# Performance work log

Measured on AMD Instinct MI355X. Metric: run time of the kernel, lower is better.

The kernel has to match this reference:

```python
import jax, jax.numpy as jnp
import numpy as np

B, S = 2, 4096
H, D = 8, 64      # num_heads, per-head embed_dim
W = 128           # window (even)
O = 64            # num_outputs per head
ZERO_VALUE = 0.0


def setup_inputs() -> dict:
    key = jax.random.key(0)
    kq, kk, kv, kwq, kwk, kbq, kbk, ko = jax.random.split(key, 8)
    scale = 1.0 / np.sqrt(D)
    return {
        "q": jax.random.normal(kq, (B, S, H * D), dtype=jnp.float32),
        "k": jax.random.normal(kk, (B, S, H * D), dtype=jnp.float32),
        "v": jax.random.normal(kv, (B, S, H * O), dtype=jnp.float32),
        "Wq": jax.random.normal(kwq, (D, D), dtype=jnp.float32) * scale,
        "bq": jax.random.normal(kbq, (D,), dtype=jnp.float32) * 0.02,
        "Wk": jax.random.normal(kwk, (D, D), dtype=jnp.float32) * scale,
        "bk": jax.random.normal(kbk, (D,), dtype=jnp.float32) * 0.02,
        "ocpe": jax.random.normal(ko, (W + 1, H), dtype=jnp.float32) * 0.02,
    }


def reference(q, k, v, Wq, bq, Wk, bk, ocpe):
    b, s, _ = q.shape
    p = W // 2
    assert s % W == 0
    C = s // W  # number of chunks of size `window`

    # split heads + per-head projections (nn.Linear: x @ W.T + b)
    q = q.reshape(b, s, H, D) @ Wq.T + bq
    k = k.reshape(b, s, H, D) @ Wk.T + bk
    v = v.reshape(b, s, H, O)

    # pad seq dim by window//2 on both sides (matches F.pad in source)
    qp = jnp.pad(q, ((0, 0), (p, p), (0, 0), (0, 0)))
    kp = jnp.pad(k, ((0, 0), (p, p), (0, 0), (0, 0)))
    vp = jnp.pad(v, ((0, 0), (p, p), (0, 0), (0, 0)))

    # overlapping chunks of length 2W (chunk_size=W plus 2*p halo)
    starts = jnp.arange(C) * W                 # (C,)
    loc = jnp.arange(2 * W)                    # (2W,)
    idx = starts[:, None] + loc[None, :]       # (C, 2W) indices into padded seq
    qc = qp[:, idx]                            # (B, C, 2W, H, D)
    kc = kp[:, idx]
    vc = vp[:, idx]                            # (B, C, 2W, H, O)

    scores = jnp.einsum('ncxhd,ncyhd->ncxyh', qc, kc)  # (B,C,2W,2W,H)

    diff = loc[None, :] - loc[:, None]         # j - i, (2W, 2W)
    within = jnp.abs(diff) <= p                # (2W, 2W)
    bias = jnp.where(within[:, :, None],
                     ocpe[jnp.clip(p + diff, 0, W)], 0.0)  # (2W,2W,H)
    scores = scores + bias[None, None]

    # boundary mask: global padded position must lie in [p, s+p)
    pos = starts[:, None] + loc[None, :]       # (C, 2W)
    valid = (pos >= p) & (pos < s + p)         # (C, 2W)
    mask = within[None] & valid[:, :, None] & valid[:, None, :]  # (C,2W,2W)

    scores = jnp.where(mask[None, :, :, :, None], scores, ZERO_VALUE)
    attn = jnp.tanh(scores)

    res = jnp.einsum('ncxyh,ncyhd->ncxd', attn, vc)  # (B,C,2W,O)
    out = res[:, :, p:2 * W - p].reshape(b, s, O)     # middle W rows per chunk

    # attn_flat[b,c,i,d,h] = attn[b,c, i+p, i+d, h]
    r = jnp.arange(W)
    rows = r[:, None] + p                      # (W, 1)
    cols = r[:, None] + jnp.arange(W + 1)[None]  # (W, W+1)
    attn_flat = attn[:, :, rows, cols, :]      # (B, C, W, W+1, H)
    attn_flat = attn_flat.reshape(b, s, W + 1, H)
    return attn_flat, out
```

## Files before the change

kernel.cpp:

```cpp
#include <hip/hip_runtime.h>
#include <cstddef>

#define SB 2
#define SS 4096
#define SH 8
#define SD 64
#define SP 64
#define SNO 129
#define TQ 16
#define WN 144
#define NT16 (SS/TQ)
#define SSTR 168

typedef _Float16 f16;
typedef __attribute__((ext_vector_type(8))) _Float16 f16x8;
typedef __attribute__((ext_vector_type(4))) float floatx4;

union f16frag { f16 h[8]; ushort4 u4[2]; f16x8 v; };
union pack4 { f16 h[4]; ushort4 u; };

__device__ __forceinline__ float fast_tanh(float x) {
  float e = __expf(2.0f * x);
  return 1.0f - 2.0f * __builtin_amdgcn_rcpf(e + 1.0f);
}

__device__ __forceinline__ void cvt16(const float* __restrict__ src, f16* __restrict__ dst) {
  float4 x0 = *(const float4*)(src);
  float4 x1 = *(const float4*)(src + 4);
  float4 x2 = *(const float4*)(src + 8);
  float4 x3 = *(const float4*)(src + 12);
  f16frag a, c;
  a.h[0]=(f16)x0.x; a.h[1]=(f16)x0.y; a.h[2]=(f16)x0.z; a.h[3]=(f16)x0.w;
  a.h[4]=(f16)x1.x; a.h[5]=(f16)x1.y; a.h[6]=(f16)x1.z; a.h[7]=(f16)x1.w;
  c.h[0]=(f16)x2.x; c.h[1]=(f16)x2.y; c.h[2]=(f16)x2.z; c.h[3]=(f16)x2.w;
  c.h[4]=(f16)x3.x; c.h[5]=(f16)x3.y; c.h[6]=(f16)x3.z; c.h[7]=(f16)x3.w;
  *(ushort4*)(dst)      = a.u4[0];
  *(ushort4*)(dst + 4)  = a.u4[1];
  *(ushort4*)(dst + 8)  = c.u4[0];
  *(ushort4*)(dst + 12) = c.u4[1];
}

__global__ __launch_bounds__(256) void prep_kernel(
    const float* __restrict__ q, const float* __restrict__ k, const float* __restrict__ v,
    const float* __restrict__ Wq, const float* __restrict__ bq,
    const float* __restrict__ Wk, const float* __restrict__ bk,
    f16* __restrict__ Qf, f16* __restrict__ Kf, f16* __restrict__ Vt)
{
  __shared__ f16 sWq[64*72], sWk[64*72], sQr[64*72], sKr[64*72], sVr[64*72];
  __shared__ float sbq[64], sbk[64];

  int t = threadIdx.x;
  int blk = blockIdx.x;
  int x = blk & 7, j = blk >> 3;
  int c = x*8 + (j & 7);
  int h = (j >> 3) & 7;
  int b = j >> 6;
  int s0 = c * 64;

  int dr = t >> 2, e0 = (t & 3) * 16;
  cvt16(Wq + dr*64 + e0, &sWq[dr*72 + e0]);
  cvt16(Wk + dr*64 + e0, &sWk[dr*72 + e0]);
  {
    size_t rbase = ((size_t)(b*SS + s0 + dr)) * (SH*SD) + h*SD + e0;
    cvt16(q + rbase, &sQr[dr*72 + e0]);
    cvt16(k + rbase, &sKr[dr*72 + e0]);
    cvt16(v + rbase, &sVr[dr*72 + e0]);
  }
  if (t < 64) { sbq[t] = bq[t]; sbk[t] = bk[t]; }
  __syncthreads();

  int lane = t & 63, wave = t >> 6;
  int r16 = lane & 15, g = lane >> 4;
  size_t hsbase = (size_t)(b*SH + h) * SS;

  #pragma unroll
  for (int jj = 0; jj < 4; ++jj) {
    int tt = wave + 4*jj;
    int si = tt >> 2, dj = tt & 3;
    floatx4 accq = {0.f,0.f,0.f,0.f}, acck = {0.f,0.f,0.f,0.f};
    #pragma unroll
    for (int e = 0; e < 64; e += 32) {
      f16x8 aq = *(const f16x8*)&sQr[(si*16 + r16)*72 + e + g*8];
      f16x8 ak = *(const f16x8*)&sKr[(si*16 + r16)*72 + e + g*8];
      f16x8 wq8 = *(const f16x8*)&sWq[(dj*16 + r16)*72 + e + g*8];
      f16x8 wk8 = *(const f16x8*)&sWk[(dj*16 + r16)*72 + e + g*8];
      accq = __builtin_amdgcn_mfma_f32_16x16x32_f16(aq, wq8, accq, 0, 0, 0);
      acck = __builtin_amdgcn_mfma_f32_16x16x32_f16(ak, wk8, acck, 0, 0, 0);
    }
    float biasq = sbq[dj*16 + r16];
    float biask = sbk[dj*16 + r16];
    #pragma unroll
    for (int rr = 0; rr < 4; ++rr) {
      int srow = s0 + si*16 + g*4 + rr;
      Qf[(hsbase + srow)*64 + dj*16 + r16] = (f16)(accq[rr] + biasq);
      Kf[(hsbase + srow)*64 + dj*16 + r16] = (f16)(acck[rr] + biask);
    }
  }
  {
    int d = t >> 2, p4 = t & 3, sc0 = p4 * 16;
    f16frag a, c2;
    #pragma unroll
    for (int j2 = 0; j2 < 8; ++j2) a.h[j2] = sVr[(sc0 + j2)*72 + d];
    #pragma unroll
    for (int j2 = 0; j2 < 8; ++j2) c2.h[j2] = sVr[(sc0 + 8 + j2)*72 + d];
    f16* dst = Vt + ((size_t)(b*SH + h)*64 + d)*SS + s0 + sc0;
    *(ushort4*)dst       = a.u4[0];
    *(ushort4*)(dst + 4) = a.u4[1];
    *(ushort4*)(dst + 8) = c2.u4[0];
    *(ushort4*)(dst + 12)= c2.u4[1];
  }
}

__global__ __launch_bounds__(512, 4) void attn_fused(
    const f16* __restrict__ Qf, const f16* __restrict__ Kf, const f16* __restrict__ Vt,
    const float* __restrict__ ocpe, float* __restrict__ af, float* __restrict__ outp)
{
  __shared__ f16 sPriv[SH][TQ*SSTR];
  __shared__ f16 sAF[TQ*SNO*SH];
  __shared__ float sObT[SH*SNO];

  int t = threadIdx.x;
  int lane = t & 63, wave = t >> 6;
  int r16 = lane & 15, g = lane >> 4;

  int blk = blockIdx.x;
  int x = blk & 7, j = blk >> 3;
  int t16 = x*32 + (j & 31);
  int b = j >> 5;
  int t0 = t16 * TQ, yg0 = t0 - SP;

  int h = wave;
  const f16* qb = Qf + ((size_t)(b*SH + h)*SS + t0 + r16)*64;
  f16x8 qa0 = *(const f16x8*)(qb + g*8);
  f16x8 qa1 = *(const f16x8*)(qb + 32 + g*8);

  for (int idx = t; idx < SNO*SH; idx += 512) {
    int o = idx >> 3, h2 = idx & 7;
    sObT[h2*SNO + o] = ocpe[idx];
  }
  f16* priv = &sPriv[wave][0];
  #pragma unroll
  for (int jj = 0; jj < 4; ++jj)
    priv[r16*SSTR + WN + g*4 + jj] = (f16)0.f;

  __syncthreads();

  const float* ob = &sObT[h*SNO];
  const f16* kbase = Kf + ((size_t)(b*SH + h)*SS)*64;
  floatx4 acc2[4] = {{0.f,0.f,0.f,0.f},{0.f,0.f,0.f,0.f},{0.f,0.f,0.f,0.f},{0.f,0.f,0.f,0.f}};

  bool interior = (t16 >= 4) & (t16 <= 250);

  if (interior) {
    const f16* krow = kbase + (size_t)(yg0 + r16) * 64 + g*8;
    #pragma unroll
    for (int yy = 0; yy < 9; ++yy) {
      f16x8 kb0 = *(const f16x8*)(krow + yy*1024);
      f16x8 kb1 = *(const f16x8*)(krow + yy*1024 + 32);
      floatx4 acc = {0.f,0.f,0.f,0.f};
      acc = __builtin_amdgcn_mfma_f32_16x16x32_f16(kb0, qa0, acc, 0, 0, 0);
      acc = __builtin_amdgcn_mfma_f32_16x16x32_f16(kb1, qa1, acc, 0, 0, 0);
      int y0 = yy*16 + g*4;
      int i = r16;
      pack4 pk;
      #pragma unroll
      for (int rr = 0; rr < 4; ++rr) {
        int o = y0 + rr - i;
        bool ook = (o >= 0) & (o <= 2*SP);
        f16 ah = (f16)0.f;
        if (ook) {
          ah = (f16)fast_tanh(acc[rr] + ob[o]);
          sAF[((size_t)i*SNO + o)*SH + h] = ah;
        }
        pk.h[rr] = ah;
      }
      *(ushort4*)&priv[i*SSTR + y0] = pk.u;
    }
    const f16* vrow = Vt + ((size_t)(b*SH + h)*64 + r16)*SS + yg0 + g*8;
    #pragma unroll
    for (int ks = 0; ks < 5; ++ks) {
      int yb = ks*32 + g*8;
      f16x8 a0 = *(const f16x8*)&priv[r16*SSTR + yb];
      #pragma unroll
      for (int dq = 0; dq < 4; ++dq) {
        f16x8 bv = *(const f16x8*)(vrow + (size_t)(dq*16)*SS + ks*32);
        acc2[dq] = __builtin_amdgcn_mfma_f32_16x16x32_f16(a0, bv, acc2[dq], 0, 0, 0);
      }
    }
  } else {
    #pragma unroll
    for (int yy = 0; yy < 9; ++yy) {
      int ldr = yg0 + yy*16 + r16;
      int ldc = min(max(ldr, 0), SS-1);
      const f16* kr = kbase + (size_t)ldc * 64;
      f16x8 kb0 = *(const f16x8*)(kr + g*8);
      f16x8 kb1 = *(const f16x8*)(kr + 32 + g*8);
      floatx4 acc = {0.f,0.f,0.f,0.f};
      acc = __builtin_amdgcn_mfma_f32_16x16x32_f16(kb0, qa0, acc, 0, 0, 0);
      acc = __builtin_amdgcn_mfma_f32_16x16x32_f16(kb1, qa1, acc, 0, 0, 0);
      int y0 = yy*16 + g*4;
      int i = r16;
      pack4 pk;
      #pragma unroll
      for (int rr = 0; rr < 4; ++rr) {
        int y = y0 + rr;
        int ygr = yg0 + y;
        int o = y - i;
        bool ok = (ygr >= 0) & (ygr < SS) & (o >= 0) & (o <= 2*SP);
        f16 ah = (f16)0.f;
        if (ok) ah = (f16)fast_tanh(acc[rr] + ob[o]);
        if ((o >= 0) & (o <= 2*SP)) sAF[((size_t)i*SNO + o)*SH + h] = ah;
        pk.h[rr] = ah;
      }
      *(ushort4*)&priv[i*SSTR + y0] = pk.u;
    }
    const f16* vb0 = Vt + ((size_t)(b*SH + h)*64 + r16)*SS;
    #pragma unroll
    for (int ks = 0; ks < 5; ++ks) {
      int yb = ks*32 + g*8;
      int ygr = yg0 + yb;
      int ygc = min(max(ygr, 0), SS-8);
      f16x8 a0 = *(const f16x8*)&priv[r16*SSTR + yb];
      #pragma unroll
      for (int dq = 0; dq < 4; ++dq) {
        f16x8 bv = *(const f16x8*)(vb0 + (size_t)(dq*16)*SS + ygc);
        acc2[dq] = __builtin_amdgcn_mfma_f32_16x16x32_f16(a0, bv, acc2[dq], 0, 0, 0);
      }
    }
  }

  {
    float* po = (float*)priv;
    #pragma unroll
    for (int dq = 0; dq < 4; ++dq)
      #pragma unroll
      for (int rr = 0; rr < 4; ++rr)
        po[(g*4 + rr)*64 + dq*16 + r16] = acc2[dq][rr];
  }

  __syncthreads();

  {
    int e2 = t * 2;
    int i = e2 >> 6, d = e2 & 63;
    float sx = 0.f, sy = 0.f;
    #pragma unroll
    for (int h2 = 0; h2 < SH; ++h2) {
      const float* ph = (const float*)&sPriv[h2][0];
      sx += ph[i*64 + d];
      sy += ph[i*64 + d + 1];
    }
    *(float2*)(outp + ((size_t)b*SS + t0 + i)*64 + d) = make_float2(sx, sy);
  }

  {
    float* afb = af + ((size_t)b*SS + t0) * (size_t)(SNO*SH);
    for (int idx = t; idx < TQ*SNO*SH/4; idx += 512) {
      const f16* s = &sAF[idx*4];
      float4 w = make_float4((float)s[0], (float)s[1], (float)s[2], (float)s[3]);
      *(float4*)(afb + idx*4) = w;
    }
  }
}

extern "C" void kernel_launch(void* const* d_in, const int* in_sizes, int n_in,
                              void* d_out, int out_size, void* d_ws, size_t ws_size,
                              hipStream_t stream) {
  const float* q    = (const float*)d_in[0];
  const float* k    = (const float*)d_in[1];
  const float* v    = (const float*)d_in[2];
  const float* Wq   = (const float*)d_in[3];
  const float* bq   = (const float*)d_in[4];
  const float* Wk   = (const float*)d_in[5];
  const float* bk   = (const float*)d_in[6];
  const float* ocpe = (const float*)d_in[7];

  f16* Kf = (f16*)d_ws;
  f16* Vt = Kf + (size_t)SB*SH*SS*SD;
  f16* Qf = Vt + (size_t)SB*SH*SS*SD;

  float* af = (float*)d_out;
  float* op = af + (size_t)SB*SS*SNO*SH;

  prep_kernel<<<SB*SH*64, 256, 0, stream>>>(q, k, v, Wq, bq, Wk, bk, Qf, Kf, Vt);
  attn_fused<<<SB*NT16, 512, 0, stream>>>(Qf, Kf, Vt, ocpe, af, op);
}
```

Measured before the change: 44.44 us.

## Split attention into per-head single-wave blocks with a separate attention-flat emit kernel

Replaces the 8-wave fused attention block with one 64-thread block per (batch, tile, head). Each block writes its f16 tanh scores tile into the attn_flat output buffer as scratch. Per-head partial outputs are accumulated with float atomicAdd into an output that the prep kernel now zeroes. A third kernel reads each scratch tile back and expands it into the interleaved fp32 attn_flat layout in place. The aim is to cut the large per-block shared memory and raise occupancy and parallelism. The cost is an extra launch, extra global round-trip traffic, atomics, and reliance on the in-place aliasing being safe.

```diff
diff --git a/kernel.cpp b/kernel.cpp
--- a/kernel.cpp
+++ b/kernel.cpp
@@ -11,6 +11,8 @@
 #define WN 144
 #define NT16 (SS/TQ)
 #define SSTR 168
+#define SWR 160
+#define CHUNK (TQ*SNO*SH)
 
 typedef _Float16 f16;
 typedef __attribute__((ext_vector_type(8))) _Float16 f16x8;
@@ -44,7 +46,8 @@
     const float* __restrict__ q, const float* __restrict__ k, const float* __restrict__ v,
     const float* __restrict__ Wq, const float* __restrict__ bq,
     const float* __restrict__ Wk, const float* __restrict__ bk,
-    f16* __restrict__ Qf, f16* __restrict__ Kf, f16* __restrict__ Vt)
+    f16* __restrict__ Qf, f16* __restrict__ Kf, f16* __restrict__ Vt,
+    float* __restrict__ outp)
 {
   __shared__ f16 sWq[64*72], sWk[64*72], sQr[64*72], sKr[64*72], sVr[64*72];
   __shared__ float sbq[64], sbk[64];
@@ -56,6 +59,8 @@
   int h = (j >> 3) & 7;
   int b = j >> 6;
   int s0 = c * 64;
+
+  *(float2*)(outp + (size_t)blk * 512 + t * 2) = make_float2(0.f, 0.f);
 
   int dr = t >> 2, e0 = (t & 3) * 16;
   cvt16(Wq + dr*64 + e0, &sWq[dr*72 + e0]);
@@ -111,42 +116,38 @@
   }
 }
 
-__global__ __launch_bounds__(512, 4) void attn_fused(
+__global__ __launch_bounds__(64, 4) void attn_bc(
     const f16* __restrict__ Qf, const f16* __restrict__ Kf, const f16* __restrict__ Vt,
-    const float* __restrict__ ocpe, float* __restrict__ af, float* __restrict__ outp)
+    const float* __restrict__ ocpe, f16* __restrict__ Sbase, float* __restrict__ outp)
 {
-  __shared__ f16 sPriv[SH][TQ*SSTR];
-  __shared__ f16 sAF[TQ*SNO*SH];
-  __shared__ float sObT[SH*SNO];
-
-  int t = threadIdx.x;
-  int lane = t & 63, wave = t >> 6;
+  __shared__ f16 sS[TQ*SSTR];
+  __shared__ float sOb[SNO];
+
+  int lane = threadIdx.x;
   int r16 = lane & 15, g = lane >> 4;
 
   int blk = blockIdx.x;
-  int x = blk & 7, j = blk >> 3;
-  int t16 = x*32 + (j & 31);
-  int b = j >> 5;
+  int x = blk & 7;
+  int idx = blk >> 3;
+  int h = idx & 7;
+  int tt = (idx >> 3) & 31;
+  int b = idx >> 8;
+  int t16 = x*32 + tt;
   int t0 = t16 * TQ, yg0 = t0 - SP;
 
-  int h = wave;
   const f16* qb = Qf + ((size_t)(b*SH + h)*SS + t0 + r16)*64;
   f16x8 qa0 = *(const f16x8*)(qb + g*8);
   f16x8 qa1 = *(const f16x8*)(qb + 32 + g*8);
 
-  for (int idx = t; idx < SNO*SH; idx += 512) {
-    int o = idx >> 3, h2 = idx & 7;
-    sObT[h2*SNO + o] = ocpe[idx];
-  }
-  f16* priv = &sPriv[wave][0];
+  for (int o = lane; o < SNO; o += 64) sOb[o] = ocpe[o*SH + h];
   #pragma unroll
   for (int jj = 0; jj < 4; ++jj)
-    priv[r16*SSTR + WN + g*4 + jj] = (f16)0.f;
-
+    sS[r16*SSTR + WN + g*4 + jj] = (f16)0.f;
   __syncthreads();
 
-  const float* ob = &sObT[h*SNO];
+  const float* ob = sOb;
   const f16* kbase = Kf + ((size_t)(b*SH + h)*SS)*64;
+  f16* stile = Sbase + (size_t)(b*NT16 + t16) * 33024 + h * (TQ*SWR);
   floatx4 acc2[4] = {{0.f,0.f,0.f,0.f},{0.f,0.f,0.f,0.f},{0.f,0.f,0.f,0.f},{0.f,0.f,0.f,0.f}};
 
   bool interior = (t16 >= 4) & (t16 <= 250);
@@ -168,19 +169,17 @@
         int o = y0 + rr - i;
         bool ook = (o >= 0) & (o <= 2*SP);
         f16 ah = (f16)0.f;
-        if (ook) {
-          ah = (f16)fast_tanh(acc[rr] + ob[o]);
-          sAF[((size_t)i*SNO + o)*SH + h] = ah;
-        }
+        if (ook) ah = (f16)fast_tanh(acc[rr] + ob[o]);
         pk.h[rr] = ah;
       }
-      *(ushort4*)&priv[i*SSTR + y0] = pk.u;
+      *(ushort4*)&sS[i*SSTR + y0] = pk.u;
+      *(ushort4*)&stile[i*SWR + y0] = pk.u;
     }
     const f16* vrow = Vt + ((size_t)(b*SH + h)*64 + r16)*SS + yg0 + g*8;
     #pragma unroll
     for (int ks = 0; ks < 5; ++ks) {
       int yb = ks*32 + g*8;
-      f16x8 a0 = *(const f16x8*)&priv[r16*SSTR + yb];
+      f16x8 a0 = *(const f16x8*)&sS[r16*SSTR + yb];
       #pragma unroll
       for (int dq = 0; dq < 4; ++dq) {
         f16x8 bv = *(const f16x8*)(vrow + (size_t)(dq*16)*SS + ks*32);
@@ -209,18 +208,17 @@
         bool ok = (ygr >= 0) & (ygr < SS) & (o >= 0) & (o <= 2*SP);
         f16 ah = (f16)0.f;
         if (ok) ah = (f16)fast_tanh(acc[rr] + ob[o]);
-        if ((o >= 0) & (o <= 2*SP)) sAF[((size_t)i*SNO + o)*SH + h] = ah;
         pk.h[rr] = ah;
       }
-      *(ushort4*)&priv[i*SSTR + y0] = pk.u;
+      *(ushort4*)&sS[i*SSTR + y0] = pk.u;
+      *(ushort4*)&stile[i*SWR + y0] = pk.u;
     }
     const f16* vb0 = Vt + ((size_t)(b*SH + h)*64 + r16)*SS;
     #pragma unroll
     for (int ks = 0; ks < 5; ++ks) {
       int yb = ks*32 + g*8;
-      int ygr = yg0 + yb;
-      int ygc = min(max(ygr, 0), SS-8);
-      f16x8 a0 = *(const f16x8*)&priv[r16*SSTR + yb];
+      int ygc = min(max(yg0 + yb, 0), SS-8);
+      f16x8 a0 = *(const f16x8*)&sS[r16*SSTR + yb];
       #pragma unroll
       for (int dq = 0; dq < 4; ++dq) {
         f16x8 bv = *(const f16x8*)(vb0 + (size_t)(dq*16)*SS + ygc);
@@ -229,36 +227,40 @@
     }
   }
 
-  {
-    float* po = (float*)priv;
-    #pragma unroll
-    for (int dq = 0; dq < 4; ++dq)
-      #pragma unroll
-      for (int rr = 0; rr < 4; ++rr)
-        po[(g*4 + rr)*64 + dq*16 + r16] = acc2[dq][rr];
-  }
-
+  #pragma unroll
+  for (int dq = 0; dq < 4; ++dq)
+    #pragma unroll
+    for (int rr = 0; rr < 4; ++rr)
+      atomicAdd(outp + ((size_t)b*SS + t0 + g*4 + rr)*64 + dq*16 + r16, acc2[dq][rr]);
+}
+
+__global__ __launch_bounds__(256) void af_emit(
+    const f16* __restrict__ Sbase, float* __restrict__ af)
+{
+  __shared__ f16 sS8[8 * TQ * SWR];
+
+  int t = threadIdx.x;
+  int t16 = blockIdx.x & 255, b = blockIdx.x >> 8;
+  const f16* src = Sbase + (size_t)(b*NT16 + t16) * 33024;
+
+  for (int idx = t; idx < 2560; idx += 256)
+    *(float4*)&sS8[idx*8] = *(const float4*)(src + (size_t)idx*8);
   __syncthreads();
 
-  {
-    int e2 = t * 2;
-    int i = e2 >> 6, d = e2 & 63;
-    float sx = 0.f, sy = 0.f;
-    #pragma unroll
-    for (int h2 = 0; h2 < SH; ++h2) {
-      const float* ph = (const float*)&sPriv[h2][0];
-      sx += ph[i*64 + d];
-      sy += ph[i*64 + d + 1];
-    }
-    *(float2*)(outp + ((size_t)b*SS + t0 + i)*64 + d) = make_float2(sx, sy);
-  }
-
-  {
-    float* afb = af + ((size_t)b*SS + t0) * (size_t)(SNO*SH);
-    for (int idx = t; idx < TQ*SNO*SH/4; idx += 512) {
-      const f16* s = &sAF[idx*4];
-      float4 w = make_float4((float)s[0], (float)s[1], (float)s[2], (float)s[3]);
-      *(float4*)(afb + idx*4) = w;
+  int i = t >> 4, o0 = t & 15;
+  const f16* srow = &sS8[i*SWR + i];
+  float* dst0 = af + ((size_t)(b*SS + t16*TQ + i) * SNO) * SH;
+  #pragma unroll
+  for (int jj = 0; jj < 9; ++jj) {
+    int o = o0 + 16*jj;
+    if (o < SNO) {
+      float v0[8];
+      #pragma unroll
+      for (int hh = 0; hh < 8; ++hh)
+        v0[hh] = (float)srow[hh*(TQ*SWR) + o];
+      float* dst = dst0 + (size_t)o*SH;
+      *(float4*)dst       = make_float4(v0[0], v0[1], v0[2], v0[3]);
+      *(float4*)(dst + 4) = make_float4(v0[4], v0[5], v0[6], v0[7]);
     }
   }
 }
@@ -281,7 +283,9 @@
 
   float* af = (float*)d_out;
   float* op = af + (size_t)SB*SS*SNO*SH;
-
-  prep_kernel<<<SB*SH*64, 256, 0, stream>>>(q, k, v, Wq, bq, Wk, bk, Qf, Kf, Vt);
-  attn_fused<<<SB*NT16, 512, 0, stream>>>(Qf, Kf, Vt, ocpe, af, op);
-}
+  f16* Sbase = (f16*)af;
+
+  prep_kernel<<<SB*SH*64, 256, 0, stream>>>(q, k, v, Wq, bq, Wk, bk, Qf, Kf, Vt, op);
+  attn_bc<<<SB*SH*NT16, 64, 0, stream>>>(Qf, Kf, Vt, ocpe, Sbase, op);
+  af_emit<<<SB*NT16, 256, 0, stream>>>(Sbase, af);
+}
```

New measurement: 64.46 us. 1.45x slower.
